# Kernel optimization log

Measured on AMD Instinct MI355X. Metric: run time of the kernel, lower is better.

## Reference

```python
import jax, jax.numpy as jnp
import numpy as np

N_NODES = 100000
N_EDGES = 1600000
D_IN = 128
D_OUT = 128
ALPHA = 0.01   # LeakyReLU negative slope
BN_EPS = 1e-5


def setup_inputs() -> dict:
    key = jax.random.key(0)
    ks = jax.random.split(key, 4)
    x = jax.random.normal(ks[0], (N_NODES, D_IN), dtype=jnp.float32)
    edge_idx = jax.random.randint(ks[1], (2, N_EDGES), 0, N_NODES, dtype=jnp.int64)
    # SAGEConv params: lin_l (neighbor path, with bias) and lin_r (root path, no bias)
    s = 1.0 / np.sqrt(D_IN)
    W_l = jax.random.uniform(ks[2], (D_OUT, D_IN), jnp.float32, -s, s)
    b_l = jnp.zeros((D_OUT,), jnp.float32)
    W_r = jax.random.uniform(ks[3], (D_OUT, D_IN), jnp.float32, -s, s)
    gamma = jnp.ones((D_OUT,), jnp.float32)
    beta = jnp.zeros((D_OUT,), jnp.float32)
    return {"x": x, "edge_idx": edge_idx, "W_l": W_l, "b_l": b_l,
            "W_r": W_r, "gamma": gamma, "beta": beta}


def reference(x, edge_idx, W_l, b_l, W_r, gamma, beta):
    src = edge_idx[0]
    dst = edge_idx[1]
    # mean aggregation of source-node features at target nodes (PyG SAGEConv default)
    msg_sum = jax.ops.segment_sum(x[src], dst, num_segments=N_NODES)      # [N, D_IN]
    cnt = jax.ops.segment_sum(jnp.ones((src.shape[0],), x.dtype), dst,
                              num_segments=N_NODES)                        # [N]
    mean = msg_sum / jnp.maximum(cnt, 1.0)[:, None]
    # out = lin_l(mean_agg) + lin_r(x)
    h = mean @ W_l.T + b_l + x @ W_r.T                                     # [N, D_OUT]
    # BatchNorm1d in training mode (biased variance over node dim)
    mu = jnp.mean(h, axis=0)
    var = jnp.mean((h - mu) ** 2, axis=0)
    h = gamma * (h - mu) * jax.lax.rsqrt(var + BN_EPS) + beta
    # LeakyReLU
    return jnp.where(h >= 0, h, ALPHA * h)
```

## Files before the change

kernel.cpp:

```cpp
#include <hip/hip_runtime.h>
#include <hip/hip_bf16.h>
#include <stdint.h>

#define N_NODES 100000
#define N_EDGES 1600000
#define DIM     128
#define ALPHA   0.01f
#define BN_EPS  1e-5f
#define NBUCK   3125
#define NBLK_P  256
#define EPB     6250
#define SRT_CAP 1536
#define BCKT_CAP 1024
#define GEMM_GRID 391

typedef __bf16 bf16x8 __attribute__((ext_vector_type(8)));
typedef float  f32x4  __attribute__((ext_vector_type(4)));
typedef float  f32x2  __attribute__((ext_vector_type(2)));

#if defined(__has_builtin)
#if __has_builtin(__builtin_amdgcn_cvt_pk_fp8_f32) && __has_builtin(__builtin_amdgcn_cvt_pk_f32_fp8)
#define USE_FP8_BUILTIN 1
#endif
#endif

static const size_t OFF_SUM   = 512;
static const size_t OFF_BT    = 14592;
static const size_t OFF_BFRAG = 6432768;
static const size_t OFF_AMEAN = 6498304;
static const size_t OFF_X8    = 32098304;
static const size_t OFF_H     = 44898304;
static const size_t OFF_GHIST = OFF_H;
static const size_t OFF_SOFFT = OFF_H + 4194304;
static const size_t OFF_TMP2  = OFF_H + 8388608;
static const size_t OFF_XB    = 70498304;

__device__ __forceinline__ float bf2f(unsigned short h) {
    return __uint_as_float(((unsigned int)h) << 16);
}
__device__ __forceinline__ float bflo(unsigned int w) {
    return __uint_as_float(w << 16);
}
__device__ __forceinline__ float bfhi(unsigned int w) {
    return __uint_as_float(w & 0xffff0000u);
}
__device__ __forceinline__ unsigned short f2bf(float f) {
    unsigned int u = __float_as_uint(f);
    u = u + 0x7fffu + ((u >> 16) & 1u);
    return (unsigned short)(u >> 16);
}
__device__ __forceinline__ unsigned int pack2(float a, float b) {
    return (unsigned int)f2bf(a) | ((unsigned int)f2bf(b) << 16);
}
__device__ __forceinline__ float loadS(const void* p, int i, int isf32) {
    return isf32 ? ((const float*)p)[i] : bf2f(((const unsigned short*)p)[i]);
}
__device__ __forceinline__ int edge_at(const void* e, long long i, int idx64) {
    return idx64 ? (int)((const long long*)e)[i] : ((const int*)e)[i];
}
__device__ __forceinline__ int blkpos(int k) { return ((k & 7) << 5) | (k >> 3); }
__device__ __forceinline__ int posblk(int p) { return ((p & 31) << 3) | (p >> 5); }

__device__ __forceinline__ void gload_lds16(const void* g, void* l) {
    __builtin_amdgcn_global_load_lds(
        reinterpret_cast<const __attribute__((address_space(1))) unsigned int*>(
            reinterpret_cast<uintptr_t>(g)),
        reinterpret_cast<__attribute__((address_space(3))) unsigned int*>(
            reinterpret_cast<uintptr_t>(l)),
        16, 0, 0);
}

#ifndef USE_FP8_BUILTIN
__device__ __forceinline__ unsigned int enc_fp8_1(float f) {
    unsigned int u = __float_as_uint(f);
    unsigned int s = (u >> 24) & 0x80u;
    unsigned int au = u & 0x7fffffffu;
    if (au >= 0x43E00000u) return s | 0x7Eu;
    if (au < 0x3C800000u) {
        int m = (int)rintf(__uint_as_float(au) * 512.0f);
        return s | (unsigned int)m;
    }
    unsigned int r = au + 0x7FFFFu + ((au >> 20) & 1u);
    unsigned int e = (r >> 23) & 0xffu;
    unsigned int m3 = (r >> 20) & 7u;
    return s | ((e - 120u) << 3) | m3;
}
#endif
__device__ __forceinline__ unsigned int enc4(float f0, float f1, float f2, float f3) {
#ifdef USE_FP8_BUILTIN
    int r = __builtin_amdgcn_cvt_pk_fp8_f32(f0, f1, 0, false);
    r = __builtin_amdgcn_cvt_pk_fp8_f32(f2, f3, r, true);
    return (unsigned int)r;
#else
    return enc_fp8_1(f0) | (enc_fp8_1(f1) << 8) | (enc_fp8_1(f2) << 16) | (enc_fp8_1(f3) << 24);
#endif
}
__device__ __forceinline__ void dec4(unsigned int w, float* o) {
#ifdef USE_FP8_BUILTIN
    f32x2 a = __builtin_amdgcn_cvt_pk_f32_fp8(w, false);
    f32x2 b = __builtin_amdgcn_cvt_pk_f32_fp8(w, true);
    o[0] = a[0]; o[1] = a[1]; o[2] = b[0]; o[3] = b[1];
#else
    #pragma unroll
    for (int j = 0; j < 4; j++) {
        unsigned int c = (w >> (8 * j)) & 0xffu;
        o[j] = __uint_as_float(((c & 0x80u) << 24) | ((c & 0x7fu) << 20)) * 0x1p120f;
    }
#endif
}

__device__ __forceinline__ int detect_idx64(const void* e) {
    const unsigned int* ew = (const unsigned int*)e;
    unsigned long long m = __ballot(ew[2 * (threadIdx.x & 63) + 1] != 0u);
    return (__popcll(m) < 8) ? 1 : 0;
}
__device__ __forceinline__ int detect_isf32(const void* x) {
    const unsigned int* xw = (const unsigned int*)x;
    unsigned int w = xw[threadIdx.x & 63];
    unsigned int e = (w >> 7) & 0xffu;
    bool bflike = (e >= 110u && e <= 140u) || ((w & 0xffffu) == 0u);
    unsigned long long m = __ballot(bflike);
    return (__popcll(m) > 32) ? 0 : 1;
}

__global__ __launch_bounds__(256) void k1_kernel(const void* edges, const void* x,
                                                 int* ghist, unsigned int* x8,
                                                 unsigned short* xb, float* gz,
                                                 const void* W_l, const void* W_r,
                                                 unsigned short* bfrag) {
    int tid = threadIdx.x;
    if (blockIdx.x < NBLK_P) {
        __shared__ int sh[NBUCK];
        int idx64 = detect_idx64(edges);
        int blk = blockIdx.x;
        if (blk == 0) gz[tid] = 0.f;
        for (int i = tid; i < NBUCK; i += 256) sh[i] = 0;
        __syncthreads();
        long long base = (long long)blk * EPB;
        for (int i = tid; i < EPB; i += 256) {
            int d = edge_at(edges, (long long)N_EDGES + base + i, idx64);
            atomicAdd(&sh[d >> 5], 1);
        }
        __syncthreads();
        for (int i = tid; i < NBUCK; i += 256) ghist[blk * NBUCK + i] = sh[i];
    } else if (blockIdx.x < NBLK_P + 3125) {
        int isf32 = detect_isf32(x);
        int gid = (blockIdx.x - NBLK_P) * 256 + tid;
        float f[16];
        if (!isf32) {
            const uint4* xv = (const uint4*)x;
            uint4 a = xv[gid * 2], b2 = xv[gid * 2 + 1];
            unsigned int w[8] = {a.x, a.y, a.z, a.w, b2.x, b2.y, b2.z, b2.w};
            #pragma unroll
            for (int i = 0; i < 8; i++) { f[2 * i] = bflo(w[i]); f[2 * i + 1] = bfhi(w[i]); }
        } else {
            const float4* xf = (const float4*)x;
            #pragma unroll
            for (int i = 0; i < 4; i++) {
                float4 v = xf[gid * 4 + i];
                f[4 * i] = v.x; f[4 * i + 1] = v.y; f[4 * i + 2] = v.z; f[4 * i + 3] = v.w;
            }
            uint4 h1, h2;
            h1.x = pack2(f[0], f[1]);  h1.y = pack2(f[2], f[3]);
            h1.z = pack2(f[4], f[5]);  h1.w = pack2(f[6], f[7]);
            h2.x = pack2(f[8], f[9]);  h2.y = pack2(f[10], f[11]);
            h2.z = pack2(f[12], f[13]); h2.w = pack2(f[14], f[15]);
            ((uint4*)xb)[gid * 2]     = h1;
            ((uint4*)xb)[gid * 2 + 1] = h2;
        }
        uint4 o;
        o.x = enc4(f[0], f[1], f[2], f[3]);
        o.y = enc4(f[4], f[5], f[6], f[7]);
        o.z = enc4(f[8], f[9], f[10], f[11]);
        o.w = enc4(f[12], f[13], f[14], f[15]);
        *(uint4*)(x8 + gid * 4) = o;
    } else {
        int isf32 = detect_isf32(x);
        int g = (blockIdx.x - NBLK_P - 3125) * 256 + tid;
        int j    = g & 7;
        int lane = (g >> 3) & 63;
        int s    = (g >> 9) & 7;
        int tt   = (g >> 12) & 7;
        int n = tt * 16 + (lane & 15);
        int k = s * 32 + ((lane >> 4) & 3) * 8 + j;
        float v = (k < DIM) ? loadS(W_l, n * DIM + k, isf32)
                            : loadS(W_r, n * DIM + (k - DIM), isf32);
        bfrag[g] = f2bf(v);
    }
}

__global__ __launch_bounds__(512) void p2a_kernel(const int* __restrict__ ghist,
                                                  int* __restrict__ sOffT,
                                                  int* __restrict__ bT) {
    __shared__ int csum[8][64];
    int t = threadIdx.x;
    int c = t >> 6, bl = t & 63;
    int b = blockIdx.x * 64 + bl;
    int v[32]; int s = 0;
    if (b < NBUCK) {
        #pragma unroll
        for (int i = 0; i < 32; i++) { v[i] = ghist[(size_t)(i * 8 + c) * NBUCK + b]; s += v[i]; }
    }
    csum[c][bl] = s;
    __syncthreads();
    if (b < NBUCK) {
        int run = 0;
        for (int i = 0; i < c; i++) run += csum[i][bl];
        #pragma unroll
        for (int i = 0; i < 32; i++) { sOffT[(size_t)(c * 32 + i) * NBUCK + b] = run; run += v[i]; }
        if (c == 7) bT[b] = run;
    }
}

__global__ __launch_bounds__(1024) void p3_kernel(const void* edges, const int* __restrict__ sOffT,
                                                  unsigned int* __restrict__ tmp) {
    __shared__ int sbase[NBUCK];
    int idx64 = detect_idx64(edges);
    int blk = blockIdx.x, tid = threadIdx.x;
    int mypos = blkpos(blk);
    for (int i = tid; i < NBUCK; i += 1024)
        sbase[i] = (i << 10) + sOffT[(size_t)mypos * NBUCK + i];
    __syncthreads();
    long long base = (long long)blk * EPB;
    for (int i = tid; i < EPB; i += 1024) {
        long long e = base + i;
        int s = edge_at(edges, e, idx64);
        int d = edge_at(edges, (long long)N_EDGES + e, idx64);
        int bkt = d >> 5;
        int p = atomicAdd(&sbase[bkt], 1);
        if (p < ((bkt + 1) << 10))
            tmp[p] = ((unsigned int)(d & 31) << 17) | (unsigned int)s;
    }
}

__global__ __launch_bounds__(256) void agg_kernel(const unsigned int* x8, const unsigned int* tmp,
                                                  const int* __restrict__ bT, unsigned short* Amean) {
    __shared__ int s_cnt[32];
    __shared__ int s_beg[32];
    __shared__ int s_srt[SRT_CAP];
    int b = blockIdx.x, tid = threadIdx.x;
    int gb = b << 10;
    int nE = min(bT[b], BCKT_CAP);
    if (tid < 32) s_cnt[tid] = 0;
    __syncthreads();
    for (int i = tid; i < nE; i += 256) atomicAdd(&s_cnt[tmp[gb + i] >> 17], 1);
    __syncthreads();
    if (tid < 32) {
        int v = s_cnt[tid];
        int sc = v;
        #pragma unroll
        for (int off = 1; off < 32; off <<= 1) {
            int u = __shfl_up(sc, off, 64);
            if (tid >= off) sc += u;
        }
        s_beg[tid] = sc - v;
        s_cnt[tid] = sc - v;
    }
    __syncthreads();
    for (int i = tid; i < nE; i += 256) {
        unsigned int w = tmp[gb + i];
        int p = atomicAdd(&s_cnt[w >> 17], 1);
        s_srt[p] = (int)(w & 0x1ffffu);
    }
    __syncthreads();
    int wv = tid >> 6, lane = tid & 63;
    int oct = lane >> 3, l8 = lane & 7;
    int nl = wv * 8 + oct;
    int nb = s_beg[nl], ne2 = s_cnt[nl];
    const uint4* xv = (const uint4*)x8;
    float acc[16];
    #pragma unroll
    for (int i = 0; i < 16; i++) acc[i] = 0.f;
    for (int jj = nb; jj < ne2; jj += 4) {
        uint4 r[4]; float mk[4];
        #pragma unroll
        for (int u = 0; u < 4; u++) {
            int e = jj + u;
            int su = s_srt[(e < ne2) ? e : nb];
            mk[u] = (e < ne2) ? 1.f : 0.f;
            r[u] = xv[(size_t)su * 8 + l8];
        }
        #pragma unroll
        for (int u = 0; u < 4; u++) {
            float f[4];
            dec4(r[u].x, f);
            acc[0] = fmaf(f[0], mk[u], acc[0]);  acc[1] = fmaf(f[1], mk[u], acc[1]);
            acc[2] = fmaf(f[2], mk[u], acc[2]);  acc[3] = fmaf(f[3], mk[u], acc[3]);
            dec4(r[u].y, f);
            acc[4] = fmaf(f[0], mk[u], acc[4]);  acc[5] = fmaf(f[1], mk[u], acc[5]);
            acc[6] = fmaf(f[2], mk[u], acc[6]);  acc[7] = fmaf(f[3], mk[u], acc[7]);
            dec4(r[u].z, f);
            acc[8] = fmaf(f[0], mk[u], acc[8]);  acc[9] = fmaf(f[1], mk[u], acc[9]);
            acc[10] = fmaf(f[2], mk[u], acc[10]); acc[11] = fmaf(f[3], mk[u], acc[11]);
            dec4(r[u].w, f);
            acc[12] = fmaf(f[0], mk[u], acc[12]); acc[13] = fmaf(f[1], mk[u], acc[13]);
            acc[14] = fmaf(f[2], mk[u], acc[14]); acc[15] = fmaf(f[3], mk[u], acc[15]);
        }
    }
    int ng = b * 32 + nl;
    float inv = 1.0f / (float)max(ne2 - nb, 1);
    uint4 o1, o2;
    o1.x = pack2(acc[0] * inv, acc[1] * inv);
    o1.y = pack2(acc[2] * inv, acc[3] * inv);
    o1.z = pack2(acc[4] * inv, acc[5] * inv);
    o1.w = pack2(acc[6] * inv, acc[7] * inv);
    o2.x = pack2(acc[8] * inv, acc[9] * inv);
    o2.y = pack2(acc[10] * inv, acc[11] * inv);
    o2.z = pack2(acc[12] * inv, acc[13] * inv);
    o2.w = pack2(acc[14] * inv, acc[15] * inv);
    *(uint4*)(Amean + (size_t)ng * 128 + l8 * 16) = o1;
    *(uint4*)(Amean + (size_t)ng * 128 + l8 * 16 + 8) = o2;
}

__global__ __launch_bounds__(256, 2) void gemm_kernel(const unsigned short* __restrict__ Amean,
                                                      const void* __restrict__ x,
                                                      const unsigned short* __restrict__ xb,
                                                      const unsigned short* __restrict__ Bfrag_g,
                                                      const void* __restrict__ b_l,
                                                      unsigned int* __restrict__ Hu,
                                                      float* __restrict__ gz) {
    __shared__ unsigned short lds[32768];
    __shared__ float sstat[2][128];
    int isf32 = detect_isf32(x);
    const unsigned short* xs = isf32 ? xb : (const unsigned short*)x;
    int tid = threadIdx.x;
    int wave = tid >> 6, lane = tid & 63;
    int lm = lane & 15, lq = lane >> 4;

    #pragma unroll
    for (int k = 0; k < 16; k++) {
        int e = tid + k * 256;
        gload_lds16(Bfrag_g + (size_t)e * 8, lds + (size_t)e * 8);
    }
    if (tid < 128) { sstat[0][tid] = 0.f; sstat[1][tid] = 0.f; }

    int base = blockIdx.x * 256;
    bf16x8 aq[4][8];
    #pragma unroll
    for (int j = 0; j < 4; j++) {
        int rowA = base + (wave * 4 + j) * 16 + lm;
        if (rowA >= N_NODES) rowA = N_NODES - 1;
        const unsigned short* am = Amean + (size_t)rowA * 128 + lq * 8;
        const unsigned short* xm = xs + (size_t)rowA * 128 + lq * 8;
        #pragma unroll
        for (int s = 0; s < 4; s++) aq[j][s] = *(const bf16x8*)(am + s * 32);
        #pragma unroll
        for (int s = 0; s < 4; s++) aq[j][4 + s] = *(const bf16x8*)(xm + s * 32);
    }
    float bv[8];
    #pragma unroll
    for (int t = 0; t < 8; t++) bv[t] = loadS(b_l, t * 16 + lm, isf32);
    float st1[8], st2[8];
    #pragma unroll
    for (int t = 0; t < 8; t++) { st1[t] = 0.f; st2[t] = 0.f; }

    __syncthreads();

    #pragma unroll
    for (int j = 0; j < 4; j++) {
        f32x4 acc[8];
        #pragma unroll
        for (int t = 0; t < 8; t++) acc[t] = (f32x4){0.f, 0.f, 0.f, 0.f};
        #pragma unroll
        for (int s = 0; s < 8; s++) {
            #pragma unroll
            for (int t = 0; t < 8; t++) {
                bf16x8 bb = *(const bf16x8*)(lds + ((t * 8 + s) * 64 + lane) * 8);
                acc[t] = __builtin_amdgcn_mfma_f32_16x16x32_bf16(aq[j][s], bb, acc[t], 0, 0, 0);
            }
        }
        #pragma unroll
        for (int t = 0; t < 8; t++) {
            #pragma unroll
            for (int r = 0; r < 4; r++) {
                int ro = base + (wave * 4 + j) * 16 + lq * 4 + r;
                float v = acc[t][r] + bv[t];
                float p = __shfl_xor(v, 1, 64);
                bool in = (ro < N_NODES);
                if (in) { st1[t] += v; st2[t] += v * v; }
                if (in && !(lm & 1)) Hu[(size_t)ro * 64 + t * 8 + (lm >> 1)] = pack2(v, p);
            }
        }
    }
    #pragma unroll
    for (int t = 0; t < 8; t++) {
        atomicAdd(&sstat[0][t * 16 + lm], st1[t]);
        atomicAdd(&sstat[1][t * 16 + lm], st2[t]);
    }
    __syncthreads();
    if (tid < 128) {
        atomicAdd(&gz[tid], sstat[0][tid]);
        atomicAdd(&gz[128 + tid], sstat[1][tid]);
    }
}

__global__ __launch_bounds__(256) void bn_norm_kernel(const unsigned int* __restrict__ Hu,
                                                      const void* x,
                                                      const float* gsum,
                                                      const float* gsumsq, const void* gamma,
                                                      const void* beta, void* out) {
    __shared__ float sc[128], sh[128];
    int isf32 = detect_isf32(x);
    int tid = threadIdx.x;
    if (tid < 128) {
        const float invN = 1.0f / (float)N_NODES;
        float mu = gsum[tid] * invN;
        float var = gsumsq[tid] * invN - mu * mu;
        float rstd = rsqrtf(var + BN_EPS);
        float g = loadS(gamma, tid, isf32);
        float b = loadS(beta, tid, isf32);
        sc[tid] = g * rstd;
        sh[tid] = b - mu * g * rstd;
    }
    __syncthreads();
    size_t idx = (size_t)blockIdx.x * 256 + tid;
    size_t i8 = idx * 8;
    float h[8];
    {
        uint4 u = *(const uint4*)(Hu + idx * 4);
        h[0]=bflo(u.x); h[1]=bfhi(u.x); h[2]=bflo(u.y); h[3]=bfhi(u.y);
        h[4]=bflo(u.z); h[5]=bfhi(u.z); h[6]=bflo(u.w); h[7]=bfhi(u.w);
    }
    int c0 = (int)(i8 & 127);
    float o[8];
    #pragma unroll
    for (int i = 0; i < 8; i++) {
        float v = h[i] * sc[c0 + i] + sh[c0 + i];
        o[i] = (v >= 0.f) ? v : ALPHA * v;
    }
    if (isf32) {
        *(float4*)((float*)out + i8) = make_float4(o[0], o[1], o[2], o[3]);
        *(float4*)((float*)out + i8 + 4) = make_float4(o[4], o[5], o[6], o[7]);
    } else {
        uint4 u;
        u.x = pack2(o[0], o[1]); u.y = pack2(o[2], o[3]);
        u.z = pack2(o[4], o[5]); u.w = pack2(o[6], o[7]);
        *(uint4*)((unsigned short*)out + i8) = u;
    }
}

extern "C" void kernel_launch(void* const* d_in, const int* in_sizes, int n_in,
                              void* d_out, int out_size, void* d_ws, size_t ws_size,
                              hipStream_t stream) {
    const void* x     = d_in[0];
    const void* eidx  = d_in[1];
    const void* W_l   = d_in[2];
    const void* b_l   = d_in[3];
    const void* W_r   = d_in[4];
    const void* gamma = d_in[5];
    const void* beta  = d_in[6];
    char* ws = (char*)d_ws;
    float* gz = (float*)(ws + OFF_SUM);
    int* bT = (int*)(ws + OFF_BT);
    unsigned short* bfrag = (unsigned short*)(ws + OFF_BFRAG);
    unsigned short* Amean = (unsigned short*)(ws + OFF_AMEAN);
    unsigned int* x8 = (unsigned int*)(ws + OFF_X8);
    unsigned int* H = (unsigned int*)(ws + OFF_H);
    unsigned short* xb = (unsigned short*)(ws + OFF_XB);
    int* ghist = (int*)(ws + OFF_GHIST);
    int* sOffT = (int*)(ws + OFF_SOFFT);
    unsigned int* tmp = (unsigned int*)(ws + OFF_TMP2);

    k1_kernel<<<NBLK_P + 3125 + 128, 256, 0, stream>>>(eidx, x, ghist, x8, xb, gz, W_l, W_r, bfrag);
    p2a_kernel<<<49, 512, 0, stream>>>(ghist, sOffT, bT);
    p3_kernel<<<NBLK_P, 1024, 0, stream>>>(eidx, sOffT, tmp);
    agg_kernel<<<NBUCK, 256, 0, stream>>>(x8, tmp, bT, Amean);
    gemm_kernel<<<GEMM_GRID, 256, 0, stream>>>(Amean, x, xb, bfrag, b_l, H, gz);
    bn_norm_kernel<<<6250, 256, 0, stream>>>(H, x, gz, gz + 128, gamma, beta, d_out);
}
```

Measured before the change: 231.6 us.

## Shrink GEMM tiles to 32 rows, stage A in swizzled LDS, spread BN atomics

The GEMM now runs one 32-row tile per block across 3125 blocks instead of 256-row tiles across 391 blocks, so work spreads over many more CUs. The A operands (mean aggregate and x) are loaded asynchronously into LDS with an XOR swizzle, and each wave covers a 16-row by 64-column sub-tile. BatchNorm partial sums go to 8 replicated accumulators in global memory, which bn_norm sums, to cut atomic contention. In exchange, every block now reloads the full 64KB B-fragment table into LDS, which greatly increases L2 traffic and per-block setup.

Result: slower. 250.2 us (+8.0%).

```diff
diff --git a/kernel.cpp b/kernel.cpp
--- a/kernel.cpp
+++ b/kernel.cpp
@@ -12,7 +12,7 @@
 #define EPB     6250
 #define SRT_CAP 1536
 #define BCKT_CAP 1024
-#define GEMM_GRID 391
+#define GEMM_GRID 3125
 
 typedef __bf16 bf16x8 __attribute__((ext_vector_type(8)));
 typedef float  f32x4  __attribute__((ext_vector_type(4)));
@@ -133,7 +133,8 @@
         __shared__ int sh[NBUCK];
         int idx64 = detect_idx64(edges);
         int blk = blockIdx.x;
-        if (blk == 0) gz[tid] = 0.f;
+        if (blk == 0)
+            for (int i = tid; i < 2048; i += 256) gz[i] = 0.f;
         for (int i = tid; i < NBUCK; i += 256) sh[i] = 0;
         __syncthreads();
         long long base = (long long)blk * EPB;
@@ -319,93 +320,103 @@
                                                       const void* __restrict__ b_l,
                                                       unsigned int* __restrict__ Hu,
                                                       float* __restrict__ gz) {
-    __shared__ unsigned short lds[32768];
-    __shared__ float sstat[2][128];
+    __shared__ unsigned short lds[40960];
     int isf32 = detect_isf32(x);
     const unsigned short* xs = isf32 ? xb : (const unsigned short*)x;
     int tid = threadIdx.x;
     int wave = tid >> 6, lane = tid & 63;
     int lm = lane & 15, lq = lane >> 4;
+    int blk = blockIdx.x;
+    int row0 = blk * 32;
 
     #pragma unroll
     for (int k = 0; k < 16; k++) {
         int e = tid + k * 256;
         gload_lds16(Bfrag_g + (size_t)e * 8, lds + (size_t)e * 8);
     }
-    if (tid < 128) { sstat[0][tid] = 0.f; sstat[1][tid] = 0.f; }
-
-    int base = blockIdx.x * 256;
-    bf16x8 aq[4][8];
-    #pragma unroll
-    for (int j = 0; j < 4; j++) {
-        int rowA = base + (wave * 4 + j) * 16 + lm;
-        if (rowA >= N_NODES) rowA = N_NODES - 1;
-        const unsigned short* am = Amean + (size_t)rowA * 128 + lq * 8;
-        const unsigned short* xm = xs + (size_t)rowA * 128 + lq * 8;
-        #pragma unroll
-        for (int s = 0; s < 4; s++) aq[j][s] = *(const bf16x8*)(am + s * 32);
-        #pragma unroll
-        for (int s = 0; s < 4; s++) aq[j][4 + s] = *(const bf16x8*)(xm + s * 32);
-    }
-    float bv[8];
-    #pragma unroll
-    for (int t = 0; t < 8; t++) bv[t] = loadS(b_l, t * 16 + lm, isf32);
-    float st1[8], st2[8];
-    #pragma unroll
-    for (int t = 0; t < 8; t++) { st1[t] = 0.f; st2[t] = 0.f; }
-
-    __syncthreads();
-
-    #pragma unroll
-    for (int j = 0; j < 4; j++) {
-        f32x4 acc[8];
-        #pragma unroll
-        for (int t = 0; t < 8; t++) acc[t] = (f32x4){0.f, 0.f, 0.f, 0.f};
-        #pragma unroll
-        for (int s = 0; s < 8; s++) {
-            #pragma unroll
-            for (int t = 0; t < 8; t++) {
-                bf16x8 bb = *(const bf16x8*)(lds + ((t * 8 + s) * 64 + lane) * 8);
-                acc[t] = __builtin_amdgcn_mfma_f32_16x16x32_bf16(aq[j][s], bb, acc[t], 0, 0, 0);
-            }
-        }
-        #pragma unroll
-        for (int t = 0; t < 8; t++) {
-            #pragma unroll
-            for (int r = 0; r < 4; r++) {
-                int ro = base + (wave * 4 + j) * 16 + lq * 4 + r;
-                float v = acc[t][r] + bv[t];
-                float p = __shfl_xor(v, 1, 64);
-                bool in = (ro < N_NODES);
-                if (in) { st1[t] += v; st2[t] += v * v; }
-                if (in && !(lm & 1)) Hu[(size_t)ro * 64 + t * 8 + (lm >> 1)] = pack2(v, p);
-            }
-        }
-    }
-    #pragma unroll
-    for (int t = 0; t < 8; t++) {
-        atomicAdd(&sstat[0][t * 16 + lm], st1[t]);
-        atomicAdd(&sstat[1][t * 16 + lm], st2[t]);
-    }
-    __syncthreads();
+    #pragma unroll
+    for (int k = 0; k < 4; k++) {
+        int La = tid + k * 256;
+        int r = La >> 5, csw = La & 31;
+        int c = csw ^ (r & 7);
+        const unsigned short* src = (c < 16)
+            ? Amean + (size_t)(row0 + r) * 128 + c * 8
+            : xs + (size_t)(row0 + r) * 128 + (c - 16) * 8;
+        gload_lds16(src, lds + 32768 + (size_t)La * 8);
+    }
+
+    int wc = wave & 1, wr = wave >> 1;
+    float bv[4];
+    #pragma unroll
+    for (int t = 0; t < 4; t++) bv[t] = loadS(b_l, (wc * 4 + t) * 16 + lm, isf32);
+
+    __syncthreads();
+
+    int rowl = wr * 16 + lm;
+    f32x4 acc[4];
+    #pragma unroll
+    for (int t = 0; t < 4; t++) acc[t] = (f32x4){0.f, 0.f, 0.f, 0.f};
+    #pragma unroll
+    for (int s = 0; s < 8; s++) {
+        bf16x8 a = *(const bf16x8*)(lds + 32768 +
+                        ((size_t)rowl * 32 + (((s << 2) | lq) ^ (rowl & 7))) * 8);
+        #pragma unroll
+        for (int t = 0; t < 4; t++) {
+            int th = wc * 4 + t;
+            bf16x8 bb = *(const bf16x8*)(lds + ((th * 8 + s) * 64 + lane) * 8);
+            acc[t] = __builtin_amdgcn_mfma_f32_16x16x32_bf16(a, bb, acc[t], 0, 0, 0);
+        }
+    }
+    float st1[4], st2[4];
+    int ro0 = row0 + wr * 16 + lq * 4;
+    #pragma unroll
+    for (int t = 0; t < 4; t++) {
+        int th = wc * 4 + t;
+        st1[t] = 0.f; st2[t] = 0.f;
+        #pragma unroll
+        for (int r = 0; r < 4; r++) {
+            int ro = ro0 + r;
+            float v = acc[t][r] + bv[t];
+            float p = __shfl_xor(v, 1, 64);
+            st1[t] += v; st2[t] += v * v;
+            if (!(lm & 1)) Hu[(size_t)ro * 64 + th * 8 + (lm >> 1)] = pack2(v, p);
+        }
+    }
+    __syncthreads();
+    float* sstat = (float*)(lds + 32768);
+    if (tid < 128) { sstat[tid] = 0.f; sstat[128 + tid] = 0.f; }
+    __syncthreads();
+    #pragma unroll
+    for (int t = 0; t < 4; t++) {
+        int col = (wc * 4 + t) * 16 + lm;
+        atomicAdd(&sstat[col], st1[t]);
+        atomicAdd(&sstat[128 + col], st2[t]);
+    }
+    __syncthreads();
+    float* gzr = gz + (size_t)(blk & 7) * 256;
     if (tid < 128) {
-        atomicAdd(&gz[tid], sstat[0][tid]);
-        atomicAdd(&gz[128 + tid], sstat[1][tid]);
+        atomicAdd(&gzr[tid], sstat[tid]);
+        atomicAdd(&gzr[128 + tid], sstat[128 + tid]);
     }
 }
 
 __global__ __launch_bounds__(256) void bn_norm_kernel(const unsigned int* __restrict__ Hu,
                                                       const void* x,
-                                                      const float* gsum,
-                                                      const float* gsumsq, const void* gamma,
+                                                      const float* gz, const void* gamma,
                                                       const void* beta, void* out) {
     __shared__ float sc[128], sh[128];
     int isf32 = detect_isf32(x);
     int tid = threadIdx.x;
     if (tid < 128) {
+        float s1 = 0.f, s2 = 0.f;
+        #pragma unroll
+        for (int i = 0; i < 8; i++) {
+            s1 += gz[i * 256 + tid];
+            s2 += gz[i * 256 + 128 + tid];
+        }
         const float invN = 1.0f / (float)N_NODES;
-        float mu = gsum[tid] * invN;
-        float var = gsumsq[tid] * invN - mu * mu;
+        float mu = s1 * invN;
+        float var = s2 * invN - mu * mu;
         float rstd = rsqrtf(var + BN_EPS);
         float g = loadS(gamma, tid, isf32);
         float b = loadS(beta, tid, isf32);
@@ -466,5 +477,5 @@
     p3_kernel<<<NBLK_P, 1024, 0, stream>>>(eidx, sOffT, tmp);
     agg_kernel<<<NBUCK, 256, 0, stream>>>(x8, tmp, bT, Amean);
     gemm_kernel<<<GEMM_GRID, 256, 0, stream>>>(Amean, x, xb, bfrag, b_l, H, gz);
-    bn_norm_kernel<<<6250, 256, 0, stream>>>(H, x, gz, gz + 128, gamma, beta, d_out);
-}
+    bn_norm_kernel<<<6250, 256, 0, stream>>>(H, x, gz, gamma, beta, d_out);
+}
```
